# Kernel tuning notes

Hardware: AMD Instinct MI355X
Metric: run time of the kernel (lower is better)

The kernel has to match this reference:

```python
import jax, jax.numpy as jnp
import numpy as np

TS = 0.1
ECNUM = 1024
CA1NUM = 1024
CA3NUM = 1024
CA3SIGMA = 5.0
TRACKLEN = 100
ACTNUM = 2
BS = 8192
CUELOC = int(0.1 * TRACKLEN)  # sensory cue injected at this step
NOISE_P = 0.04 * TS           # per-step EC3 spontaneous-spike probability


def _xavier_std(fan_in, fan_out):
    return float(np.sqrt(2.0 / (fan_in + fan_out)))


def setup_inputs() -> dict:
    key = jax.random.key(0)
    ks = jax.random.split(key, 6)
    cue = jax.random.normal(ks[0], (BS, ECNUM), jnp.float32)
    ec5_init = jax.random.uniform(ks[1], (BS, ECNUM), jnp.float32)
    wca3ca1 = jax.random.uniform(ks[2], (CA3NUM, CA1NUM), jnp.float32) * 0.01
    wec3ca1 = jax.random.normal(ks[3], (ECNUM, CA1NUM), jnp.float32) * _xavier_std(ECNUM, CA1NUM)
    wca1ec5 = jax.random.normal(ks[4], (CA1NUM, ECNUM), jnp.float32) * _xavier_std(CA1NUM, ECNUM)
    wca1act = jax.random.normal(ks[5], (CA1NUM, ACTNUM), jnp.float32) * _xavier_std(CA1NUM, ACTNUM)
    ca1bias = jnp.zeros((CA1NUM,), jnp.float32)
    ec5bias = jnp.zeros((ECNUM,), jnp.float32)
    actbias = jnp.zeros((ACTNUM,), jnp.float32)
    return {"cue": cue, "ec5_init": ec5_init, "wca3ca1": wca3ca1,
            "wec3ca1": wec3ca1, "wca1ec5": wca1ec5, "wca1act": wca1act,
            "ca1bias": ca1bias, "ec5bias": ec5bias, "actbias": actbias}


def _forward(cue, ec5_init, wca3ca1, wec3ca1, wca1ec5, wca1act, ca1bias, ec5bias, actbias):
    bs = cue.shape[0]
    dt = cue.dtype
    # CA3 place-cell tuning curves for all positions: (T, ca3num)
    ca3center = jnp.linspace(0.0, TRACKLEN, CA3NUM).astype(dt)
    xs = jnp.arange(TRACKLEN)
    ca3_all = jnp.exp(-((ca3center[None, :] - xs[:, None].astype(dt)) ** 2)
                      / (2.0 * CA3SIGMA ** 2))
    drive = ca3_all @ wca3ca1            # (T, ca1num), precomputed CA3->CA1 drive
    cue_mask = (xs == CUELOC).astype(dt)  # (T,)
    noise_key = jax.random.key(42)

    ec3_0 = jnp.zeros((bs, ECNUM), dt)
    ca1_0 = jnp.zeros((bs, CA1NUM), dt)

    def step(carry, inp):
        ec3, ec5, _ = carry
        d, m, t = inp
        ca1 = jax.nn.relu(d[None, :] * (1.0 + jax.nn.sigmoid(ec3 @ wec3ca1)) - ca1bias)
        ec5 = ec5 + (10.0 * TS) * (ca1 @ wca1ec5) + ec5bias
        ec5 = 0.5 + 0.5 * jax.nn.sigmoid(4.0 * (ec5 - 0.5))
        ec3 = ec5 * ec3 + m * cue
        k = jax.random.fold_in(noise_key, t)
        ec3 = ec3 + 0.2 * jax.random.bernoulli(k, NOISE_P, (bs, ECNUM)).astype(dt)
        return (ec3, ec5, ca1), None

    (ec3, ec5, ca1), _ = jax.lax.scan(step, (ec3_0, ec5_init, ca1_0),
                                      (drive, cue_mask, xs))
    return ca1 @ wca1act + actbias       # (bs, actnum)


def reference(cue, ec5_init, wca3ca1, wec3ca1, wca1ec5, wca1act, ca1bias, ec5bias, actbias):
    return _forward(cue, ec5_init, wca3ca1, wec3ca1, wca1ec5, wca1act,
                    ca1bias, ec5bias, actbias)
```

## Files before the change

### kernel.cpp

```cpp
#include <hip/hip_runtime.h>
#include <stdint.h>

#define BS 8192
#define NDIM 1024
#define T_STEPS 100
#define CUE_T 10
#define BK 64
#define NKT (NDIM / BK)

typedef __attribute__((ext_vector_type(8))) short bf16x8;
typedef __attribute__((ext_vector_type(16))) float f32x16;

__device__ inline uint16_t f32_to_bf16(float f) {
    uint32_t u = __float_as_uint(f);
    uint32_t r = u + 0x7fffu + ((u >> 16) & 1u);
    return (uint16_t)(r >> 16);
}
__device__ inline float bf16_to_f32(uint16_t h) {
    return __uint_as_float(((uint32_t)h) << 16);
}

__host__ __device__ inline uint32_t rotl32_(uint32_t x, uint32_t r) {
    return (x << r) | (x >> (32u - r));
}

__host__ __device__ inline void tf2x32(uint32_t k0, uint32_t k1,
                                       uint32_t x0, uint32_t x1,
                                       uint32_t &o0, uint32_t &o1) {
    uint32_t ks2 = k0 ^ k1 ^ 0x1BD11BDAu;
    x0 += k0; x1 += k1;
#define TF_R4(a,b,c,d) \
    x0 += x1; x1 = rotl32_(x1,(a)); x1 ^= x0; \
    x0 += x1; x1 = rotl32_(x1,(b)); x1 ^= x0; \
    x0 += x1; x1 = rotl32_(x1,(c)); x1 ^= x0; \
    x0 += x1; x1 = rotl32_(x1,(d)); x1 ^= x0;
    TF_R4(13,15,26,6)  x0 += k1;  x1 += ks2 + 1u;
    TF_R4(17,29,16,24) x0 += ks2; x1 += k0 + 2u;
    TF_R4(13,15,26,6)  x0 += k0;  x1 += k1 + 3u;
    TF_R4(17,29,16,24) x0 += k1;  x1 += ks2 + 4u;
    TF_R4(13,15,26,6)  x0 += ks2; x1 += k0 + 5u;
#undef TF_R4
    o0 = x0; o1 = x1;
}

__device__ inline float sigmoidf_(float x) {
    return 1.0f / (1.0f + expf(-x));
}

__device__ __forceinline__ void gload16(const uint16_t* g, uint16_t* l) {
    __builtin_amdgcn_global_load_lds(
        (const __attribute__((address_space(1))) void*)g,
        (__attribute__((address_space(3))) void*)l, 16, 0, 0);
}

__global__ void init_kernel(const float* __restrict__ ec5_init,
                            uint16_t* __restrict__ ec3bf,
                            uint16_t* __restrict__ ec5bf, int n) {
    int i = blockIdx.x * blockDim.x + threadIdx.x;
    if (i < n) { ec3bf[i] = 0; ec5bf[i] = f32_to_bf16(ec5_init[i]); }
}

__global__ __launch_bounds__(256) void drive_kernel(const float* __restrict__ W,
                                                    float* __restrict__ drive) {
    __shared__ float g[4][1024];
    const int t0 = blockIdx.x * 4;
    const int c = blockIdx.y * 256 + threadIdx.x;
    const float stepf = 100.0f / 1023.0f;
    for (int i = threadIdx.x; i < 4096; i += 256) {
        int tt = i >> 10, j = i & 1023;
        float d = stepf * (float)j - (float)(t0 + tt);
        g[tt][j] = expf(-(d * d) * 0.02f);
    }
    __syncthreads();
    float a0 = 0.f, a1 = 0.f, a2 = 0.f, a3 = 0.f;
    for (int j = 0; j < 1024; ++j) {
        float w = W[(size_t)j * NDIM + c];
        a0 = fmaf(g[0][j], w, a0);
        a1 = fmaf(g[1][j], w, a1);
        a2 = fmaf(g[2][j], w, a2);
        a3 = fmaf(g[3][j], w, a3);
    }
    drive[(size_t)(t0 + 0) * NDIM + c] = a0;
    drive[(size_t)(t0 + 1) * NDIM + c] = a1;
    drive[(size_t)(t0 + 2) * NDIM + c] = a2;
    drive[(size_t)(t0 + 3) * NDIM + c] = a3;
}

__global__ __launch_bounds__(256) void wtrans_kernel(const float* __restrict__ W,
                                                     uint16_t* __restrict__ Wt) {
    __shared__ float tile[32][33];
    int k0 = blockIdx.x * 32, n0 = blockIdx.y * 32;
    int tx = threadIdx.x & 31, ty = threadIdx.x >> 5;
    #pragma unroll
    for (int i = 0; i < 32; i += 8)
        tile[ty + i][tx] = W[(size_t)(k0 + ty + i) * NDIM + n0 + tx];
    __syncthreads();
    #pragma unroll
    for (int i = 0; i < 32; i += 8)
        Wt[(size_t)(n0 + ty + i) * NDIM + k0 + tx] = f32_to_bf16(tile[tx][ty + i]);
}

template<bool NOISE>
__device__ __forceinline__ void gemm_core_t(const uint16_t* __restrict__ A,
                                            const uint16_t* __restrict__ Bt,
                                            uint16_t* As, uint16_t* Bs,
                                            f32x16 acc[2][2],
                                            uint32_t k0_, uint32_t k1_,
                                            uint32_t obase, uint64_t &mask) {
    const int tid = threadIdx.x;
    const int wid = tid >> 6, lane = tid & 63;
    const int row0 = blockIdx.x * 128, col0 = blockIdx.y * 128;
    const int srow = lane >> 3;
    const int soff = ((lane & 7) ^ srow) * 8;
    const uint16_t* aS[4]; const uint16_t* bS[4];
    #pragma unroll
    for (int i = 0; i < 4; ++i) {
        int ch = wid * 4 + i;
        aS[i] = A  + (size_t)(row0 + ch * 8 + srow) * NDIM + soff;
        bS[i] = Bt + (size_t)(col0 + ch * 8 + srow) * NDIM + soff;
    }
    const int l31 = lane & 31, l5 = lane >> 5;
    const int wr = wid >> 1, wc = wid & 1;
    int aoff[2][4], boff[2][4];
    #pragma unroll
    for (int m = 0; m < 2; ++m)
        #pragma unroll
        for (int kk = 0; kk < 4; ++kk) {
            int ar = wr * 64 + m * 32 + l31;
            aoff[m][kk] = ar * BK + ((((kk << 1) | l5) ^ (ar & 7)) << 3);
            int br = wc * 64 + m * 32 + l31;
            boff[m][kk] = br * BK + ((((kk << 1) | l5) ^ (br & 7)) << 3);
        }

    #pragma unroll
    for (int i = 0; i < 4; ++i) {
        int ch = wid * 4 + i;
        gload16(aS[i], As + ch * 512);
        gload16(bS[i], Bs + ch * 512);
    }

    for (int kt = 0; kt < NKT; ++kt) {
        const int cur = kt & 1;
        if (kt + 1 < NKT) {
            const int nb = (cur ^ 1) * 8192;
            const int k0n = (kt + 1) * BK;
            #pragma unroll
            for (int i = 0; i < 4; ++i) {
                int ch = wid * 4 + i;
                gload16(aS[i] + k0n, As + nb + ch * 512);
                gload16(bS[i] + k0n, Bs + nb + ch * 512);
            }
            asm volatile("s_waitcnt vmcnt(8)" ::: "memory");
        } else {
            asm volatile("s_waitcnt vmcnt(0)" ::: "memory");
        }
        __builtin_amdgcn_s_barrier();
        __builtin_amdgcn_sched_barrier(0);
        const uint16_t* as = As + cur * 8192;
        const uint16_t* bs = Bs + cur * 8192;
        bf16x8 af[2][4], bfr[2][4];
        #pragma unroll
        for (int m = 0; m < 2; ++m)
            #pragma unroll
            for (int kk = 0; kk < 4; ++kk) {
                af[m][kk]  = *(const bf16x8*)&as[aoff[m][kk]];
                bfr[m][kk] = *(const bf16x8*)&bs[boff[m][kk]];
            }
        #pragma unroll
        for (int kk = 0; kk < 4; ++kk)
            #pragma unroll
            for (int m = 0; m < 2; ++m)
                #pragma unroll
                for (int n = 0; n < 2; ++n)
                    acc[m][n] = __builtin_amdgcn_mfma_f32_32x32x16_bf16(
                        af[m][kk], bfr[n][kk], acc[m][n], 0, 0, 0);
        if (NOISE) {
            #pragma unroll
            for (int u = 0; u < 4; ++u) {
                int e = (kt << 2) + u;
                uint32_t off = obase + (uint32_t)((e >> 3) << 14) + (uint32_t)(e & 7);
                uint32_t o0, o1;
                tf2x32(k0_, k1_, 0u, off, o0, o1);
                uint32_t bits = o0 ^ o1;
                float uu = __uint_as_float((bits >> 9) | 0x3f800000u) - 1.0f;
                mask |= (uint64_t)(uu < 0.004f ? 1u : 0u) << e;
            }
        }
        __builtin_amdgcn_sched_barrier(0);
        __builtin_amdgcn_s_barrier();
    }
}

__device__ __forceinline__ void acc_to_lds(float* lacc, f32x16 acc[2][2]) {
    const int tid = threadIdx.x, wid = tid >> 6, lane = tid & 63;
    const int wr = wid >> 1, wc = wid & 1, l31 = lane & 31, l5 = lane >> 5;
    #pragma unroll
    for (int m = 0; m < 2; ++m)
        #pragma unroll
        for (int n = 0; n < 2; ++n) {
            int c = wc * 64 + n * 32 + l31;
            int chunk = c >> 2, cj = c & 3;
            #pragma unroll
            for (int e = 0; e < 16; ++e) {
                int r = wr * 64 + m * 32 + (e & 3) + ((e >> 2) << 3) + (l5 << 2);
                lacc[r * 128 + ((chunk ^ (r & 31)) << 2) + cj] = acc[m][n][e];
            }
        }
}

__device__ __forceinline__ void acc_read8(const float* lacc, int r, int a,
                                          float4 &v0, float4 &v1) {
    int rb = r & 31;
    v0 = *(const float4*)&lacc[r * 128 + ((((a << 1) | 0) ^ rb) << 2)];
    v1 = *(const float4*)&lacc[r * 128 + ((((a << 1) | 1) ^ rb) << 2)];
}

__global__ __launch_bounds__(256, 2) void gemm1_kernel(
    const uint16_t* __restrict__ ec3bf, const uint16_t* __restrict__ W1t,
    const float* __restrict__ drv, const float* __restrict__ bias,
    uint16_t* __restrict__ ca1bf)
{
    __shared__ __align__(16) uint16_t SM[2][16384];
    uint16_t* As = SM[0];
    uint16_t* Bs = SM[1];
    f32x16 acc[2][2];
    #pragma unroll
    for (int m = 0; m < 2; ++m)
        #pragma unroll
        for (int n = 0; n < 2; ++n)
            acc[m][n] = (f32x16)(0.0f);
    uint64_t dummy = 0;
    gemm_core_t<false>(ec3bf, W1t, As, Bs, acc, 0u, 0u, 0u, dummy);

    float* lacc = (float*)SM;
    acc_to_lds(lacc, acc);
    __syncthreads();

    const int tid = threadIdx.x;
    const int row0 = blockIdx.x * 128, col0 = blockIdx.y * 128;
    const int a = tid & 15;
    #pragma unroll
    for (int i = 0; i < 8; ++i) {
        int r = (tid >> 4) + i * 16;
        float4 v0, v1;
        acc_read8(lacc, r, a, v0, v1);
        int gc = col0 + a * 8;
        float4 d0 = *(const float4*)&drv[gc];
        float4 d1 = *(const float4*)&drv[gc + 4];
        float4 b0 = *(const float4*)&bias[gc];
        float4 b1 = *(const float4*)&bias[gc + 4];
        size_t off = (size_t)(row0 + r) * NDIM + gc;
        bf16x8 pk;
        #pragma unroll
        for (int j = 0; j < 8; ++j) {
            float accv = j < 4 ? v0[j] : v1[j - 4];
            float dv = j < 4 ? d0[j] : d1[j - 4];
            float bi = j < 4 ? b0[j] : b1[j - 4];
            float s = sigmoidf_(accv);
            float v = dv * (1.0f + s) - bi;
            v = v > 0.0f ? v : 0.0f;
            pk[j] = (short)f32_to_bf16(v);
        }
        *(bf16x8*)&ca1bf[off] = pk;
    }
}

__global__ __launch_bounds__(256, 2) void gemm2_kernel(
    const uint16_t* __restrict__ ca1bf, const uint16_t* __restrict__ W2t,
    const float* __restrict__ cue, const float* __restrict__ bias,
    uint16_t* __restrict__ ec3bf, uint16_t* __restrict__ ec5bf,
    uint32_t k0_, uint32_t k1_, int inject)
{
    __shared__ __align__(16) uint16_t SM[2][16384];
    uint16_t* As = SM[0];
    uint16_t* Bs = SM[1];
    f32x16 acc[2][2];
    #pragma unroll
    for (int m = 0; m < 2; ++m)
        #pragma unroll
        for (int n = 0; n < 2; ++n)
            acc[m][n] = (f32x16)(0.0f);

    const int tid = threadIdx.x;
    const int row0 = blockIdx.x * 128, col0 = blockIdx.y * 128;
    const int a = tid & 15;
    const uint32_t obase = (uint32_t)(row0 + (tid >> 4)) * NDIM
                         + (uint32_t)(col0 + a * 8);
    uint64_t mask = 0;
    gemm_core_t<true>(ca1bf, W2t, As, Bs, acc, k0_, k1_, obase, mask);

    bf16x8 e3v[8], e5v[8];
    #pragma unroll
    for (int i = 0; i < 8; ++i) {
        size_t off = (size_t)(row0 + (tid >> 4) + i * 16) * NDIM + col0 + a * 8;
        e3v[i] = *(const bf16x8*)&ec3bf[off];
        e5v[i] = *(const bf16x8*)&ec5bf[off];
    }

    float* lacc = (float*)SM;
    acc_to_lds(lacc, acc);
    __syncthreads();

    #pragma unroll
    for (int i = 0; i < 8; ++i) {
        int r = (tid >> 4) + i * 16;
        float4 v0, v1;
        acc_read8(lacc, r, a, v0, v1);
        int gc = col0 + a * 8;
        size_t off = (size_t)(row0 + r) * NDIM + gc;
        float4 b0 = *(const float4*)&bias[gc];
        float4 b1 = *(const float4*)&bias[gc + 4];
        float4 c0 = {0.f,0.f,0.f,0.f}, c1 = {0.f,0.f,0.f,0.f};
        if (inject) {
            c0 = *(const float4*)&cue[off];
            c1 = *(const float4*)&cue[off + 4];
        }
        bf16x8 p3, p5;
        #pragma unroll
        for (int j = 0; j < 8; ++j) {
            float accv = j < 4 ? v0[j] : v1[j - 4];
            float bi = j < 4 ? b0[j] : b1[j - 4];
            float e5 = bf16_to_f32((uint16_t)e5v[i][j]);
            float e3 = bf16_to_f32((uint16_t)e3v[i][j]);
            float u = e5 + accv + bi;
            float e5n = 0.5f + 0.5f * sigmoidf_(4.0f * (u - 0.5f));
            float e3n = e5n * e3;
            if (inject) e3n += (j < 4 ? c0[j] : c1[j - 4]);
            e3n += ((mask >> (i * 8 + j)) & 1ull) ? 0.2f : 0.0f;
            p5[j] = (short)f32_to_bf16(e5n);
            p3[j] = (short)f32_to_bf16(e3n);
        }
        *(bf16x8*)&ec5bf[off] = p5;
        *(bf16x8*)&ec3bf[off] = p3;
    }
}

__global__ __launch_bounds__(256) void final_kernel(
    const uint16_t* __restrict__ ca1bf,
    const float* __restrict__ wact,
    const float* __restrict__ actbias,
    float* __restrict__ out)
{
    int wave = threadIdx.x >> 6, lane = threadIdx.x & 63;
    int b = blockIdx.x * 4 + wave;
    double a0 = 0.0, a1 = 0.0;
    #pragma unroll
    for (int ch = 0; ch < 2; ++ch) {
        int c0 = ch * 512 + lane * 8;
        bf16x8 v = *(const bf16x8*)&ca1bf[(size_t)b * NDIM + c0];
        #pragma unroll
        for (int k = 0; k < 8; ++k) {
            double vf = (double)bf16_to_f32((uint16_t)v[k]);
            a0 += vf * (double)wact[(c0 + k) * 2 + 0];
            a1 += vf * (double)wact[(c0 + k) * 2 + 1];
        }
    }
    #pragma unroll
    for (int off = 32; off > 0; off >>= 1) {
        a0 += __shfl_down(a0, off);
        a1 += __shfl_down(a1, off);
    }
    if (lane == 0) {
        out[(size_t)b * 2 + 0] = (float)(a0 + (double)actbias[0]);
        out[(size_t)b * 2 + 1] = (float)(a1 + (double)actbias[1]);
    }
}

extern "C" void kernel_launch(void* const* d_in, const int* in_sizes, int n_in,
                              void* d_out, int out_size, void* d_ws, size_t ws_size,
                              hipStream_t stream) {
    const float* cue      = (const float*)d_in[0];
    const float* ec5_init = (const float*)d_in[1];
    const float* wca3ca1  = (const float*)d_in[2];
    const float* wec3ca1  = (const float*)d_in[3];
    const float* wca1ec5  = (const float*)d_in[4];
    const float* wca1act  = (const float*)d_in[5];
    const float* ca1bias  = (const float*)d_in[6];
    const float* ec5bias  = (const float*)d_in[7];
    const float* actbias  = (const float*)d_in[8];
    float* out = (float*)d_out;

    const size_t NE = (size_t)BS * NDIM;
    char* p = (char*)d_ws;
    uint16_t* ec3bf = (uint16_t*)p;   p += NE * 2;
    uint16_t* ec5bf = (uint16_t*)p;   p += NE * 2;
    uint16_t* ca1bf = (uint16_t*)p;   p += NE * 2;
    uint16_t* W1t   = (uint16_t*)p;   p += (size_t)NDIM * NDIM * 2;
    uint16_t* W2t   = (uint16_t*)p;   p += (size_t)NDIM * NDIM * 2;
    float*    drive = (float*)p;

    const int n = (int)NE;
    hipLaunchKernelGGL(init_kernel, dim3((n + 255) / 256), dim3(256), 0, stream,
                       ec5_init, ec3bf, ec5bf, n);
    hipLaunchKernelGGL(drive_kernel, dim3(25, 4), dim3(256), 0, stream,
                       wca3ca1, drive);
    hipLaunchKernelGGL(wtrans_kernel, dim3(32, 32), dim3(256), 0, stream, wec3ca1, W1t);
    hipLaunchKernelGGL(wtrans_kernel, dim3(32, 32), dim3(256), 0, stream, wca1ec5, W2t);

    dim3 blk(256);
    dim3 gg(BS / 128, NDIM / 128);
    for (int t = 0; t < T_STEPS; ++t) {
        hipLaunchKernelGGL(gemm1_kernel, gg, blk, 0, stream,
                           ec3bf, W1t, drive + (size_t)t * NDIM, ca1bias, ca1bf);
        if (t < T_STEPS - 1) {
            uint32_t k0, k1;
            tf2x32(0u, 42u, 0u, (uint32_t)t, k0, k1);
            hipLaunchKernelGGL(gemm2_kernel, gg, blk, 0, stream,
                               ca1bf, W2t, cue, ec5bias, ec3bf, ec5bf, k0, k1,
                               (t == CUE_T) ? 1 : 0);
        }
    }
    hipLaunchKernelGGL(final_kernel, dim3(BS / 4), blk, 0, stream,
                       ca1bf, wca1act, actbias, out);
}
```

Baseline: 6.991 ms.

## Use fast sigmoid intrinsics, keep final CA1 in fp32, re-split drive kernel

Sigmoid now uses the fast __expf and the hardware reciprocal in place of the precise expf and a divide, which shortens the epilogues of both per-step GEMMs. On the last step gemm1 also writes CA1 in fp32, and the final projection reads that instead of the bf16 copy, which is mainly an accuracy change. The drive kernel is split so each thread computes one time step over 64 columns, giving a larger grid. The fast intrinsics trade some accuracy, and the extra fp32 buffer adds one large write on the final step.

New measurement: 6.390 ms. -8.6%, faster.

```diff
diff --git a/kernel.cpp b/kernel.cpp
--- a/kernel.cpp
+++ b/kernel.cpp
@@ -44,7 +44,8 @@
 }
 
 __device__ inline float sigmoidf_(float x) {
-    return 1.0f / (1.0f + expf(-x));
+    float e = __expf(-x);
+    return __builtin_amdgcn_rcpf(1.0f + e);
 }
 
 __device__ __forceinline__ void gload16(const uint16_t* g, uint16_t* l) {
@@ -64,26 +65,19 @@
                                                     float* __restrict__ drive) {
     __shared__ float g[4][1024];
     const int t0 = blockIdx.x * 4;
-    const int c = blockIdx.y * 256 + threadIdx.x;
+    const int c = blockIdx.y * 64 + (threadIdx.x & 63);
+    const int tt = threadIdx.x >> 6;
     const float stepf = 100.0f / 1023.0f;
     for (int i = threadIdx.x; i < 4096; i += 256) {
-        int tt = i >> 10, j = i & 1023;
-        float d = stepf * (float)j - (float)(t0 + tt);
-        g[tt][j] = expf(-(d * d) * 0.02f);
+        int t_ = i >> 10, j = i & 1023;
+        float d = stepf * (float)j - (float)(t0 + t_);
+        g[t_][j] = expf(-(d * d) * 0.02f);
     }
     __syncthreads();
-    float a0 = 0.f, a1 = 0.f, a2 = 0.f, a3 = 0.f;
-    for (int j = 0; j < 1024; ++j) {
-        float w = W[(size_t)j * NDIM + c];
-        a0 = fmaf(g[0][j], w, a0);
-        a1 = fmaf(g[1][j], w, a1);
-        a2 = fmaf(g[2][j], w, a2);
-        a3 = fmaf(g[3][j], w, a3);
-    }
-    drive[(size_t)(t0 + 0) * NDIM + c] = a0;
-    drive[(size_t)(t0 + 1) * NDIM + c] = a1;
-    drive[(size_t)(t0 + 2) * NDIM + c] = a2;
-    drive[(size_t)(t0 + 3) * NDIM + c] = a3;
+    float a = 0.f;
+    for (int j = 0; j < 1024; ++j)
+        a = fmaf(g[tt][j], W[(size_t)j * NDIM + c], a);
+    drive[(size_t)(t0 + tt) * NDIM + c] = a;
 }
 
 __global__ __launch_bounds__(256) void wtrans_kernel(const float* __restrict__ W,
@@ -218,7 +212,7 @@
 __global__ __launch_bounds__(256, 2) void gemm1_kernel(
     const uint16_t* __restrict__ ec3bf, const uint16_t* __restrict__ W1t,
     const float* __restrict__ drv, const float* __restrict__ bias,
-    uint16_t* __restrict__ ca1bf)
+    uint16_t* __restrict__ ca1bf, float* __restrict__ ca1f, int writef32)
 {
     __shared__ __align__(16) uint16_t SM[2][16384];
     uint16_t* As = SM[0];
@@ -250,7 +244,7 @@
         float4 b0 = *(const float4*)&bias[gc];
         float4 b1 = *(const float4*)&bias[gc + 4];
         size_t off = (size_t)(row0 + r) * NDIM + gc;
-        bf16x8 pk;
+        float vout[8];
         #pragma unroll
         for (int j = 0; j < 8; ++j) {
             float accv = j < 4 ? v0[j] : v1[j - 4];
@@ -258,10 +252,18 @@
             float bi = j < 4 ? b0[j] : b1[j - 4];
             float s = sigmoidf_(accv);
             float v = dv * (1.0f + s) - bi;
-            v = v > 0.0f ? v : 0.0f;
-            pk[j] = (short)f32_to_bf16(v);
-        }
+            vout[j] = v > 0.0f ? v : 0.0f;
+        }
+        bf16x8 pk;
+        #pragma unroll
+        for (int j = 0; j < 8; ++j) pk[j] = (short)f32_to_bf16(vout[j]);
         *(bf16x8*)&ca1bf[off] = pk;
+        if (writef32) {
+            float4 f0 = {vout[0], vout[1], vout[2], vout[3]};
+            float4 f1 = {vout[4], vout[5], vout[6], vout[7]};
+            *(float4*)&ca1f[off] = f0;
+            *(float4*)&ca1f[off + 4] = f1;
+        }
     }
 }
 
@@ -336,7 +338,7 @@
 }
 
 __global__ __launch_bounds__(256) void final_kernel(
-    const uint16_t* __restrict__ ca1bf,
+    const float* __restrict__ ca1,
     const float* __restrict__ wact,
     const float* __restrict__ actbias,
     float* __restrict__ out)
@@ -344,16 +346,10 @@
     int wave = threadIdx.x >> 6, lane = threadIdx.x & 63;
     int b = blockIdx.x * 4 + wave;
     double a0 = 0.0, a1 = 0.0;
-    #pragma unroll
-    for (int ch = 0; ch < 2; ++ch) {
-        int c0 = ch * 512 + lane * 8;
-        bf16x8 v = *(const bf16x8*)&ca1bf[(size_t)b * NDIM + c0];
-        #pragma unroll
-        for (int k = 0; k < 8; ++k) {
-            double vf = (double)bf16_to_f32((uint16_t)v[k]);
-            a0 += vf * (double)wact[(c0 + k) * 2 + 0];
-            a1 += vf * (double)wact[(c0 + k) * 2 + 1];
-        }
+    for (int c = lane; c < NDIM; c += 64) {
+        double v = (double)ca1[(size_t)b * NDIM + c];
+        a0 += v * (double)wact[c * 2 + 0];
+        a1 += v * (double)wact[c * 2 + 1];
     }
     #pragma unroll
     for (int off = 32; off > 0; off >>= 1) {
@@ -382,6 +378,7 @@
 
     const size_t NE = (size_t)BS * NDIM;
     char* p = (char*)d_ws;
+    float*    ca1f  = (float*)p;      p += NE * 4;
     uint16_t* ec3bf = (uint16_t*)p;   p += NE * 2;
     uint16_t* ec5bf = (uint16_t*)p;   p += NE * 2;
     uint16_t* ca1bf = (uint16_t*)p;   p += NE * 2;
@@ -392,7 +389,7 @@
     const int n = (int)NE;
     hipLaunchKernelGGL(init_kernel, dim3((n + 255) / 256), dim3(256), 0, stream,
                        ec5_init, ec3bf, ec5bf, n);
-    hipLaunchKernelGGL(drive_kernel, dim3(25, 4), dim3(256), 0, stream,
+    hipLaunchKernelGGL(drive_kernel, dim3(25, 16), dim3(256), 0, stream,
                        wca3ca1, drive);
     hipLaunchKernelGGL(wtrans_kernel, dim3(32, 32), dim3(256), 0, stream, wec3ca1, W1t);
     hipLaunchKernelGGL(wtrans_kernel, dim3(32, 32), dim3(256), 0, stream, wca1ec5, W2t);
@@ -401,7 +398,8 @@
     dim3 gg(BS / 128, NDIM / 128);
     for (int t = 0; t < T_STEPS; ++t) {
         hipLaunchKernelGGL(gemm1_kernel, gg, blk, 0, stream,
-                           ec3bf, W1t, drive + (size_t)t * NDIM, ca1bias, ca1bf);
+                           ec3bf, W1t, drive + (size_t)t * NDIM, ca1bias,
+                           ca1bf, ca1f, (t == T_STEPS - 1) ? 1 : 0);
         if (t < T_STEPS - 1) {
             uint32_t k0, k1;
             tf2x32(0u, 42u, 0u, (uint32_t)t, k0, k1);
@@ -411,5 +409,5 @@
         }
     }
     hipLaunchKernelGGL(final_kernel, dim3(BS / 4), blk, 0, stream,
-                       ca1bf, wca1act, actbias, out);
-}
+                       ca1f, wca1act, actbias, out);
+}
```
